# Performance work log

Measured on AMD Instinct MI355X. Metric: run time of the kernel, lower is better.

## Reference

```python
import jax, jax.numpy as jnp
import numpy as np

N = 100_000       # nodes
DEG = 16          # avg degree (fixed here)
E = N * DEG       # edges
IN_F, HID, OUT_F = 64, 32, 16
K, DIM = 3, 2     # n_kernels, pseudo-coordinate dim


def setup_inputs() -> dict:
    key = jax.random.key(0)
    k1, k2, k3, k4, k5, k6, k7 = jax.random.split(key, 7)
    row_ptr = jnp.arange(N + 1, dtype=jnp.int64) * DEG          # CSR offsets, fixed degree
    col_idx = jax.random.randint(k1, (E,), 0, N, dtype=jnp.int64)
    input_feature = jax.random.normal(k2, (N, IN_F), dtype=jnp.float32)
    p = jax.random.uniform(k3, (E, DIM), dtype=jnp.float32)      # pseudo-coordinates per edge
    mu = jax.random.normal(k4, (K, DIM), dtype=jnp.float32)
    sigma = jax.random.uniform(k5, (K, DIM), dtype=jnp.float32, minval=0.5, maxval=1.5)
    W1 = jax.random.normal(k6, (K, IN_F, HID), dtype=jnp.float32) * (1.0 / np.sqrt(IN_F))
    W2 = jax.random.normal(k7, (K, HID, OUT_F), dtype=jnp.float32) * (1.0 / np.sqrt(HID))
    return {"row_ptr": row_ptr, "col_idx": col_idx, "input_feature": input_feature,
            "p": p, "mu": mu, "sigma": sigma, "W1": W1, "W2": W2}


def _edge_gaussians(p, mu, sigma):
    # w[e,k] = exp(-0.5 * sum_d ((p[e,d]-mu[k,d])/sigma[k,d])^2)   [E,K]
    diff = p[:, None, :] - mu[None, :, :]                 # [E,K,D]
    inv_var = 1.0 / (sigma * sigma)                       # [K,D]
    return jnp.exp(-0.5 * jnp.sum(diff * diff * inv_var[None], axis=-1))


def _gmm_conv(row_ptr, col_idx, dst, x, gauss, W):
    # per-kernel linear transform first (dense GEMM), then irregular gather+scatter
    xW = jnp.einsum('nf,kfh->nkh', x, W)                  # [N,K,H]
    msg = jnp.einsum('ek,ekh->eh', gauss, xW[col_idx])    # gather + mix kernels  [E,H]
    n_nodes = row_ptr.shape[0] - 1
    return jax.ops.segment_sum(msg, dst, num_segments=n_nodes)  # scatter-add to dst rows


def reference(row_ptr, col_idx, input_feature, p, mu, sigma, W1, W2):
    n_nodes = row_ptr.shape[0] - 1
    deg = jnp.diff(row_ptr)
    dst = jnp.repeat(jnp.arange(n_nodes), deg, total_repeat_length=col_idx.shape[0])
    gauss = _edge_gaussians(p, mu, sigma)                 # shared by both layers
    h = _gmm_conv(row_ptr, col_idx, dst, input_feature, gauss, W1)
    out = _gmm_conv(row_ptr, col_idx, dst, h, gauss, W2)
    return out
```

## Files before the change

### kernel.cpp

```cpp
#include <hip/hip_runtime.h>
#include <hip/hip_fp16.h>


#define KK 3

using half8   = __attribute__((ext_vector_type(8))) _Float16;
using float4v = __attribute__((ext_vector_type(4))) float;

__global__ void setup_kernel(const float* __restrict__ p, const float* __restrict__ mu,
                             const float* __restrict__ sigma, float2* __restrict__ gaussh,
                             const float* __restrict__ x, __half* __restrict__ xh,
                             const float* __restrict__ W1, const float* __restrict__ W2,
                             __half* __restrict__ B1, __half* __restrict__ B2,
                             int E, int NX8) {
    int t = blockIdx.x * blockDim.x + threadIdx.x;
    if (t < E) {
        float p0 = p[2 * t], p1 = p[2 * t + 1];
        float g[KK];
#pragma unroll
        for (int k = 0; k < KK; ++k) {
            float m0 = mu[2 * k], m1 = mu[2 * k + 1];
            float s0 = sigma[2 * k], s1 = sigma[2 * k + 1];
            float d0 = p0 - m0, d1 = p1 - m1;
            float q = (d0 * d0) / (s0 * s0) + (d1 * d1) / (s1 * s1);
            g[k] = __expf(-0.5f * q);
        }
        union { __half h[4]; float2 v; } o;
        o.h[0] = __float2half(g[0]); o.h[1] = __float2half(g[1]);
        o.h[2] = __float2half(g[2]); o.h[3] = __float2half(0.f);
        gaussh[t] = o.v;
    }
    if (t < NX8) {
        float4 v0 = ((const float4*)x)[2 * t];
        float4 v1 = ((const float4*)x)[2 * t + 1];
        union { __half h[8]; float4 v; } o;
        o.h[0] = __float2half(v0.x); o.h[1] = __float2half(v0.y);
        o.h[2] = __float2half(v0.z); o.h[3] = __float2half(v0.w);
        o.h[4] = __float2half(v1.x); o.h[5] = __float2half(v1.y);
        o.h[6] = __float2half(v1.z); o.h[7] = __float2half(v1.w);
        ((float4*)xh)[t] = o.v;
    }
    if (t < 6144) {
        int j = t & 7, lane = (t >> 3) & 63, grp = t >> 9;
        int ot = grp / 6, kb = grp % 6;
        int kidx = kb * 32 + (lane >> 4) * 8 + j;
        B1[t] = __float2half(W1[kidx * 32 + ot * 16 + (lane & 15)]);
    } else if (t < 6144 + 1536) {
        int t2 = t - 6144;
        int j = t2 & 7, lane = (t2 >> 3) & 63, kb = t2 >> 9;
        int kidx = kb * 32 + (lane >> 4) * 8 + j;
        B2[t2] = __float2half(W2[kidx * 16 + (lane & 15)]);
    }
}

__device__ __forceinline__ void unpack8(float4 raw, float* f) {
    union { float4 v; __half2 h2[4]; } u;
    u.v = raw;
#pragma unroll
    for (int q = 0; q < 4; ++q) {
        float2 t = __half22float2(u.h2[q]);
        f[2 * q] = t.x; f[2 * q + 1] = t.y;
    }
}

template <int F, int H, bool OUT_HALF>
__global__ __launch_bounds__(256) void fused_layer(
    const int* __restrict__ row_ptr, const int* __restrict__ col_idx,
    const float2* __restrict__ gaussh, const __half* __restrict__ xh,
    const __half* __restrict__ Bpack, void* __restrict__ yout, int N) {
    constexpr int TPN    = F / 8;
    constexpr int NODES  = 256 / TPN;
    constexpr int J      = KK * F;
    constexpr int STRIDE = (F == 64) ? 200 : 104;
    constexpr int KB     = J / 32;
    constexpr int OT     = H / 16;

    __shared__ __align__(16) __half sLh[NODES * STRIDE];

    const int tid = threadIdx.x;
    const int nl  = tid / TPN;
    const int ch  = tid % TPN;
    const int n   = blockIdx.x * NODES + nl;

    float a0[8], a1[8], a2[8];
#pragma unroll
    for (int q = 0; q < 8; ++q) { a0[q] = 0.f; a1[q] = 0.f; a2[q] = 0.f; }

    const float4* x4 = (const float4*)xh;

    if (n < N) {
        int e0 = row_ptr[n], e1 = row_ptr[n + 1];
        int e = e0;
        for (; e + 8 <= e1; e += 8) {
            int cols[8];
            float2 gr[8];
            float4 xr[8];
#pragma unroll
            for (int j = 0; j < 8; ++j) cols[j] = col_idx[e + j];
#pragma unroll
            for (int j = 0; j < 8; ++j) gr[j] = gaussh[e + j];
#pragma unroll
            for (int j = 0; j < 8; ++j) xr[j] = x4[(size_t)cols[j] * TPN + ch];
#pragma unroll
            for (int j = 0; j < 8; ++j) {
                union { float2 v; __half2 h2[2]; } ug; ug.v = gr[j];
                float2 gab = __half22float2(ug.h2[0]);
                float2 gc_ = __half22float2(ug.h2[1]);
                float f[8];
                unpack8(xr[j], f);
#pragma unroll
                for (int q = 0; q < 8; ++q) {
                    a0[q] = fmaf(gab.x, f[q], a0[q]);
                    a1[q] = fmaf(gab.y, f[q], a1[q]);
                    a2[q] = fmaf(gc_.x, f[q], a2[q]);
                }
            }
        }
        for (; e < e1; ++e) {
            int c = col_idx[e];
            union { float2 v; __half2 h2[2]; } ug; ug.v = gaussh[e];
            float2 gab = __half22float2(ug.h2[0]);
            float2 gc_ = __half22float2(ug.h2[1]);
            float f[8];
            unpack8(x4[(size_t)c * TPN + ch], f);
#pragma unroll
            for (int q = 0; q < 8; ++q) {
                a0[q] = fmaf(gab.x, f[q], a0[q]);
                a1[q] = fmaf(gab.y, f[q], a1[q]);
                a2[q] = fmaf(gc_.x, f[q], a2[q]);
            }
        }
    }

    {
        union { __half h[8]; half8 v; } o;
#pragma unroll
        for (int q = 0; q < 8; ++q) o.h[q] = __float2half(a0[q]);
        *(half8*)(sLh + nl * STRIDE + 0 * F + ch * 8) = o.v;
#pragma unroll
        for (int q = 0; q < 8; ++q) o.h[q] = __float2half(a1[q]);
        *(half8*)(sLh + nl * STRIDE + 1 * F + ch * 8) = o.v;
#pragma unroll
        for (int q = 0; q < 8; ++q) o.h[q] = __float2half(a2[q]);
        *(half8*)(sLh + nl * STRIDE + 2 * F + ch * 8) = o.v;
    }
    __syncthreads();

    {
        const int wv   = tid >> 6;
        const int lane = tid & 63;
        const int tile = wv / OT;
        const int ot   = wv % OT;
        const int n0   = blockIdx.x * NODES + tile * 16;
        if (n0 < N) {
            const int quad = lane >> 4;
            const int m    = lane & 15;

            half8 b[KB];
#pragma unroll
            for (int kb = 0; kb < KB; ++kb)
                b[kb] = ((const half8*)Bpack)[(ot * KB + kb) * 64 + lane];

            const half8* av = (const half8*)(sLh + (size_t)(tile * 16 + m) * STRIDE);
            float4v acc = {0.f, 0.f, 0.f, 0.f};
#pragma unroll
            for (int kb = 0; kb < KB; ++kb)
                acc = __builtin_amdgcn_mfma_f32_16x16x32_f16(av[kb * 4 + quad], b[kb], acc, 0, 0, 0);

#pragma unroll
            for (int reg = 0; reg < 4; ++reg) {
                int nn = n0 + quad * 4 + reg;
                if (nn < N) {
                    if constexpr (OUT_HALF)
                        ((__half*)yout)[(size_t)nn * H + ot * 16 + m] = __float2half(acc[reg]);
                    else
                        ((float*)yout)[(size_t)nn * H + m] = acc[reg];
                }
            }
        }
    }
}

extern "C" void kernel_launch(void* const* d_in, const int* in_sizes, int n_in,
                              void* d_out, int out_size, void* d_ws, size_t ws_size,
                              hipStream_t stream) {
    const int* row_ptr  = (const int*)d_in[0];
    const int* col_idx  = (const int*)d_in[1];
    const float* x      = (const float*)d_in[2];
    const float* p      = (const float*)d_in[3];
    const float* mu     = (const float*)d_in[4];
    const float* sigma  = (const float*)d_in[5];
    const float* W1     = (const float*)d_in[6];
    const float* W2     = (const float*)d_in[7];

    const int N = in_sizes[0] - 1;
    const int E = in_sizes[1];

    float2* gaussh = (float2*)d_ws;
    __half* B1pack = (__half*)(gaussh + (size_t)E);
    __half* B2pack = B1pack + 6144;
    __half* xh     = B2pack + 1536;
    __half* hh     = xh + (size_t)N * 64;
    float*  out    = (float*)d_out;

    const int B = 256;
    const int NX8 = N * 8;
    int setup_n = E > NX8 ? E : NX8;
    if (setup_n < 7680) setup_n = 7680;

    setup_kernel<<<(setup_n + B - 1) / B, B, 0, stream>>>(
        p, mu, sigma, gaussh, x, xh, W1, W2, B1pack, B2pack, E, NX8);

    fused_layer<64, 32, true><<<(N + 31) / 32, B, 0, stream>>>(
        row_ptr, col_idx, gaussh, xh, B1pack, (void*)hh, N);
    fused_layer<32, 16, false><<<(N + 63) / 64, B, 0, stream>>>(
        row_ptr, col_idx, gaussh, hh, B2pack, (void*)out, N);
}
```

Baseline: 156.2 us.

## Merge setup and both layers into one persistent kernel with grid barriers

```diff
diff --git a/kernel.cpp b/kernel.cpp
--- a/kernel.cpp
+++ b/kernel.cpp
@@ -3,55 +3,10 @@
 
 
 #define KK 3
+#define NBLK 1024
 
 using half8   = __attribute__((ext_vector_type(8))) _Float16;
 using float4v = __attribute__((ext_vector_type(4))) float;
-
-__global__ void setup_kernel(const float* __restrict__ p, const float* __restrict__ mu,
-                             const float* __restrict__ sigma, float2* __restrict__ gaussh,
-                             const float* __restrict__ x, __half* __restrict__ xh,
-                             const float* __restrict__ W1, const float* __restrict__ W2,
-                             __half* __restrict__ B1, __half* __restrict__ B2,
-                             int E, int NX8) {
-    int t = blockIdx.x * blockDim.x + threadIdx.x;
-    if (t < E) {
-        float p0 = p[2 * t], p1 = p[2 * t + 1];
-        float g[KK];
-#pragma unroll
-        for (int k = 0; k < KK; ++k) {
-            float m0 = mu[2 * k], m1 = mu[2 * k + 1];
-            float s0 = sigma[2 * k], s1 = sigma[2 * k + 1];
-            float d0 = p0 - m0, d1 = p1 - m1;
-            float q = (d0 * d0) / (s0 * s0) + (d1 * d1) / (s1 * s1);
-            g[k] = __expf(-0.5f * q);
-        }
-        union { __half h[4]; float2 v; } o;
-        o.h[0] = __float2half(g[0]); o.h[1] = __float2half(g[1]);
-        o.h[2] = __float2half(g[2]); o.h[3] = __float2half(0.f);
-        gaussh[t] = o.v;
-    }
-    if (t < NX8) {
-        float4 v0 = ((const float4*)x)[2 * t];
-        float4 v1 = ((const float4*)x)[2 * t + 1];
-        union { __half h[8]; float4 v; } o;
-        o.h[0] = __float2half(v0.x); o.h[1] = __float2half(v0.y);
-        o.h[2] = __float2half(v0.z); o.h[3] = __float2half(v0.w);
-        o.h[4] = __float2half(v1.x); o.h[5] = __float2half(v1.y);
-        o.h[6] = __float2half(v1.z); o.h[7] = __float2half(v1.w);
-        ((float4*)xh)[t] = o.v;
-    }
-    if (t < 6144) {
-        int j = t & 7, lane = (t >> 3) & 63, grp = t >> 9;
-        int ot = grp / 6, kb = grp % 6;
-        int kidx = kb * 32 + (lane >> 4) * 8 + j;
-        B1[t] = __float2half(W1[kidx * 32 + ot * 16 + (lane & 15)]);
-    } else if (t < 6144 + 1536) {
-        int t2 = t - 6144;
-        int j = t2 & 7, lane = (t2 >> 3) & 63, kb = t2 >> 9;
-        int kidx = kb * 32 + (lane >> 4) * 8 + j;
-        B2[t2] = __float2half(W2[kidx * 16 + (lane & 15)]);
-    }
-}
 
 __device__ __forceinline__ void unpack8(float4 raw, float* f) {
     union { float4 v; __half2 h2[4]; } u;
@@ -63,11 +18,24 @@
     }
 }
 
+__device__ __forceinline__ void grid_sync_phase(int* bar, int phase) {
+    __syncthreads();
+    if (threadIdx.x == 0) {
+        __threadfence();
+        __hip_atomic_fetch_add(bar, 1, __ATOMIC_RELEASE, __HIP_MEMORY_SCOPE_AGENT);
+        const int target = phase * NBLK;
+        while (__hip_atomic_load(bar, __ATOMIC_RELAXED, __HIP_MEMORY_SCOPE_AGENT) < target)
+            __builtin_amdgcn_s_sleep(8);
+        __threadfence();
+    }
+    __syncthreads();
+}
+
 template <int F, int H, bool OUT_HALF>
-__global__ __launch_bounds__(256) void fused_layer(
-    const int* __restrict__ row_ptr, const int* __restrict__ col_idx,
+__device__ __forceinline__ void fused_tile(
+    int bb, const int* __restrict__ row_ptr, const int* __restrict__ col_idx,
     const float2* __restrict__ gaussh, const __half* __restrict__ xh,
-    const __half* __restrict__ Bpack, void* __restrict__ yout, int N) {
+    const __half* __restrict__ Bpack, void* __restrict__ yout, int N, __half* sLh) {
     constexpr int TPN    = F / 8;
     constexpr int NODES  = 256 / TPN;
     constexpr int J      = KK * F;
@@ -75,12 +43,10 @@
     constexpr int KB     = J / 32;
     constexpr int OT     = H / 16;
 
-    __shared__ __align__(16) __half sLh[NODES * STRIDE];
-
     const int tid = threadIdx.x;
     const int nl  = tid / TPN;
     const int ch  = tid % TPN;
-    const int n   = blockIdx.x * NODES + nl;
+    const int n   = bb * NODES + nl;
 
     float a0[8], a1[8], a2[8];
 #pragma unroll
@@ -91,18 +57,18 @@
     if (n < N) {
         int e0 = row_ptr[n], e1 = row_ptr[n + 1];
         int e = e0;
-        for (; e + 8 <= e1; e += 8) {
-            int cols[8];
-            float2 gr[8];
-            float4 xr[8];
-#pragma unroll
-            for (int j = 0; j < 8; ++j) cols[j] = col_idx[e + j];
-#pragma unroll
-            for (int j = 0; j < 8; ++j) gr[j] = gaussh[e + j];
-#pragma unroll
-            for (int j = 0; j < 8; ++j) xr[j] = x4[(size_t)cols[j] * TPN + ch];
-#pragma unroll
-            for (int j = 0; j < 8; ++j) {
+        for (; e + 4 <= e1; e += 4) {
+            int cols[4];
+            float2 gr[4];
+            float4 xr[4];
+#pragma unroll
+            for (int j = 0; j < 4; ++j) cols[j] = col_idx[e + j];
+#pragma unroll
+            for (int j = 0; j < 4; ++j) gr[j] = gaussh[e + j];
+#pragma unroll
+            for (int j = 0; j < 4; ++j) xr[j] = x4[(size_t)cols[j] * TPN + ch];
+#pragma unroll
+            for (int j = 0; j < 4; ++j) {
                 union { float2 v; __half2 h2[2]; } ug; ug.v = gr[j];
                 float2 gab = __half22float2(ug.h2[0]);
                 float2 gc_ = __half22float2(ug.h2[1]);
@@ -151,7 +117,7 @@
         const int lane = tid & 63;
         const int tile = wv / OT;
         const int ot   = wv % OT;
-        const int n0   = blockIdx.x * NODES + tile * 16;
+        const int n0   = bb * NODES + tile * 16;
         if (n0 < N) {
             const int quad = lane >> 4;
             const int m    = lane & 15;
@@ -178,6 +144,76 @@
                 }
             }
         }
+    }
+    __syncthreads();
+}
+
+__global__ __launch_bounds__(256, 4) void mono_kernel(
+    const int* __restrict__ row_ptr, const int* __restrict__ col_idx,
+    const float* __restrict__ x, const float* __restrict__ p,
+    const float* __restrict__ mu, const float* __restrict__ sigma,
+    const float* __restrict__ W1, const float* __restrict__ W2,
+    int* bar, float2* __restrict__ gaussh, __half* __restrict__ xh,
+    __half* __restrict__ B1, __half* __restrict__ B2,
+    __half* __restrict__ hh, float* __restrict__ out, int N, int E) {
+    __shared__ __align__(16) __half sLh[6656];
+
+    {
+        const int NX8 = N * 8;
+        int total = E > NX8 ? E : NX8;
+        for (int t = blockIdx.x * 256 + threadIdx.x; t < total; t += NBLK * 256) {
+            if (t < E) {
+                float p0 = p[2 * t], p1 = p[2 * t + 1];
+                float g[KK];
+#pragma unroll
+                for (int k = 0; k < KK; ++k) {
+                    float m0 = mu[2 * k], m1 = mu[2 * k + 1];
+                    float s0 = sigma[2 * k], s1 = sigma[2 * k + 1];
+                    float d0 = p0 - m0, d1 = p1 - m1;
+                    float q = (d0 * d0) / (s0 * s0) + (d1 * d1) / (s1 * s1);
+                    g[k] = __expf(-0.5f * q);
+                }
+                union { __half h[4]; float2 v; } o;
+                o.h[0] = __float2half(g[0]); o.h[1] = __float2half(g[1]);
+                o.h[2] = __float2half(g[2]); o.h[3] = __float2half(0.f);
+                gaussh[t] = o.v;
+            }
+            if (t < NX8) {
+                float4 v0 = ((const float4*)x)[2 * t];
+                float4 v1 = ((const float4*)x)[2 * t + 1];
+                union { __half h[8]; float4 v; } o;
+                o.h[0] = __float2half(v0.x); o.h[1] = __float2half(v0.y);
+                o.h[2] = __float2half(v0.z); o.h[3] = __float2half(v0.w);
+                o.h[4] = __float2half(v1.x); o.h[5] = __float2half(v1.y);
+                o.h[6] = __float2half(v1.z); o.h[7] = __float2half(v1.w);
+                ((float4*)xh)[t] = o.v;
+            }
+            if (t < 6144) {
+                int j = t & 7, lane = (t >> 3) & 63, grp = t >> 9;
+                int ot = grp / 6, kb = grp % 6;
+                int kidx = kb * 32 + (lane >> 4) * 8 + j;
+                B1[t] = __float2half(W1[kidx * 32 + ot * 16 + (lane & 15)]);
+            } else if (t < 6144 + 1536) {
+                int t2 = t - 6144;
+                int j = t2 & 7, lane = (t2 >> 3) & 63, kb = t2 >> 9;
+                int kidx = kb * 32 + (lane >> 4) * 8 + j;
+                B2[t2] = __float2half(W2[kidx * 16 + (lane & 15)]);
+            }
+        }
+    }
+    grid_sync_phase(bar, 1);
+
+    {
+        int ntiles = (N + 31) / 32;
+        for (int bb = blockIdx.x; bb < ntiles; bb += NBLK)
+            fused_tile<64, 32, true>(bb, row_ptr, col_idx, gaussh, xh, B1, (void*)hh, N, sLh);
+    }
+    grid_sync_phase(bar, 2);
+
+    {
+        int ntiles = (N + 63) / 64;
+        for (int bb = blockIdx.x; bb < ntiles; bb += NBLK)
+            fused_tile<32, 16, false>(bb, row_ptr, col_idx, gaussh, hh, B2, (void*)out, N, sLh);
     }
 }
 
@@ -193,26 +229,19 @@
     const float* W1     = (const float*)d_in[6];
     const float* W2     = (const float*)d_in[7];
 
-    const int N = in_sizes[0] - 1;
-    const int E = in_sizes[1];
-
-    float2* gaussh = (float2*)d_ws;
+    int N = in_sizes[0] - 1;
+    int E = in_sizes[1];
+
+    int*    bar    = (int*)d_ws;
+    float2* gaussh = (float2*)((char*)d_ws + 16);
     __half* B1pack = (__half*)(gaussh + (size_t)E);
     __half* B2pack = B1pack + 6144;
     __half* xh     = B2pack + 1536;
     __half* hh     = xh + (size_t)N * 64;
     float*  out    = (float*)d_out;
 
-    const int B = 256;
-    const int NX8 = N * 8;
-    int setup_n = E > NX8 ? E : NX8;
-    if (setup_n < 7680) setup_n = 7680;
-
-    setup_kernel<<<(setup_n + B - 1) / B, B, 0, stream>>>(
-        p, mu, sigma, gaussh, x, xh, W1, W2, B1pack, B2pack, E, NX8);
-
-    fused_layer<64, 32, true><<<(N + 31) / 32, B, 0, stream>>>(
-        row_ptr, col_idx, gaussh, xh, B1pack, (void*)hh, N);
-    fused_layer<32, 16, false><<<(N + 63) / 64, B, 0, stream>>>(
-        row_ptr, col_idx, gaussh, hh, B2pack, (void*)out, N);
-}
+    hipMemsetAsync(bar, 0, 16, stream);
+    mono_kernel<<<NBLK, 256, 0, stream>>>(
+        row_ptr, col_idx, x, p, mu, sigma, W1, W2,
+        bar, gaussh, xh, B1pack, B2pack, hh, out, N, E);
+}
```

New measurement: 455.0 us. 191% more time.
